# Kernel optimization log

Hardware: AMD Instinct MI355X
Metric: run time of the kernel (lower is better)

The kernel has to match this reference:

```python
import jax, jax.numpy as jnp
import numpy as np


def phi(x):
    return jax.nn.elu(x) + 1.0


def setup_inputs() -> dict:
    key = jax.random.key(0)
    ks = jax.random.split(key, 6)
    B, C, H, W = 16, 256, 64, 64
    scale = 1.0 / np.sqrt(C)
    x = jax.random.normal(ks[0], (B, C, H, W), dtype=jnp.float32)
    Wq = jax.random.normal(ks[1], (C, C), dtype=jnp.float32) * scale
    Wk = jax.random.normal(ks[2], (C, C), dtype=jnp.float32) * scale
    Wv = jax.random.normal(ks[3], (C, C), dtype=jnp.float32) * scale
    Wo = jax.random.normal(ks[4], (C, C), dtype=jnp.float32) * scale
    bo = jnp.zeros((C,), dtype=jnp.float32)
    return {"x": x, "Wq": Wq, "Wk": Wk, "Wv": Wv, "Wo": Wo, "bo": bo}


def reference(x, Wq, Wk, Wv, Wo, bo):
    # 1x1 convs == channel matmuls: out[b,o,h,w] = sum_c W[o,c] x[b,c,h,w]
    q = jnp.einsum('oc,bchw->bohw', Wq, x)
    k = jnp.einsum('oc,bchw->bohw', Wk, x)
    v = jnp.einsum('oc,bchw->bohw', Wv, x)
    phi_q, phi_k, phi_v = phi(q), phi(k), phi(v)
    # context matrix per batch: [B, C, C]
    qv = jnp.einsum('bchw,bdhw->bcd', phi_q, phi_v)
    # per-batch 1x1 conv with weight qv[b] applied to phi_k[b]
    attended = jnp.einsum('bcd,bdhw->bchw', qv, phi_k)
    # output projection with bias; dropout is identity at eval
    out = jnp.einsum('oc,bchw->bohw', Wo, attended) + bo[None, :, None, None]
    return out
```

## Files before the change

### kernel.cpp

```cpp
#include <hip/hip_runtime.h>
#include <hip/hip_bf16.h>


typedef short  bf16x8 __attribute__((ext_vector_type(8)));
typedef float  f32x4  __attribute__((ext_vector_type(4)));
typedef unsigned short u16x4 __attribute__((ext_vector_type(4)));

#define NB 16
#define NC 256
#define NN 4096

__device__ __forceinline__ unsigned short f2bf(float f) {
    union { float f; unsigned u; } v; v.f = f;
    unsigned r = v.u + 0x7FFFu + ((v.u >> 16) & 1u);
    return (unsigned short)(r >> 16);
}

__device__ __forceinline__ float phi_act(float v) {
    return v > 0.f ? v + 1.f : __expf(v);
}

__device__ __forceinline__ void gload_lds16(const void* g, void* l) {
    __builtin_amdgcn_global_load_lds(
        (const __attribute__((address_space(1))) void*)g,
        (__attribute__((address_space(3))) void*)l, 16, 0, 0);
}

__device__ __forceinline__ void stage_tile(
    const unsigned short* __restrict__ src, int ld, int kb, char* lds, int t)
{
    const int kslot  = t & 7;
    const int rbase  = t >> 3;
    const int srcOff = (kslot * 16) ^ ((rbase & 7) << 4);
    const int wbase  = (t >> 6) * 1024;
    #pragma unroll
    for (int i = 0; i < 4; ++i) {
        const int r = i * 32 + rbase;
        const char* g = (const char*)(src + (size_t)r * ld + kb) + srcOff;
        gload_lds16(g, lds + i * 4096 + wbase);
    }
}

__device__ __forceinline__ bf16x8 frag_ld(const char* lds, int row, int kbyte) {
    return *(const bf16x8*)(lds + row * 128 + (kbyte ^ ((row & 7) << 4)));
}

template<bool SWAP>
__device__ __forceinline__ void gemm_projx(
    const unsigned short* __restrict__ A,
    const float* __restrict__ xb,
    char* lsA, char* lsB, f32x4 (&acc)[4][4])
{
    const int t = threadIdx.x, lane = t & 63, w = t >> 6;
    const int wr = (w >> 1) * 64, wc = (w & 1) * 64;
    const int q = lane >> 4, c15 = lane & 15;
    const int cb = t & 15;
    const int nb0 = t >> 4;

    for (int kt = 0; kt < 4; ++kt) {
        const int kb = kt * 64;
        f32x4 bv[2][4];
        #pragma unroll
        for (int i = 0; i < 2; ++i) {
            const float* src = xb + (size_t)(kb + cb * 4) * NN + (nb0 + 16 * i) * 4;
            #pragma unroll
            for (int j = 0; j < 4; ++j)
                bv[i][j] = *(const f32x4*)(src + (size_t)j * NN);
        }
        if (kt) __syncthreads();
        stage_tile(A, NC, kb, lsA, t);
        #pragma unroll
        for (int i = 0; i < 2; ++i) {
            const int nb = nb0 + 16 * i;
            #pragma unroll
            for (int jj = 0; jj < 4; ++jj) {
                const int n = nb * 4 + jj;
                u16x4 wv;
                #pragma unroll
                for (int j = 0; j < 4; ++j) wv[j] = f2bf(bv[i][j][jj]);
                *(u16x4*)(lsB + n * 128 + ((cb * 8) ^ ((n & 7) << 4))) = wv;
            }
        }
        __syncthreads();
        #pragma unroll
        for (int g = 0; g < 2; ++g) {
            const int kbyte = g * 64 + q * 16;
            bf16x8 af[4], bfr[4];
            #pragma unroll
            for (int m = 0; m < 4; ++m) af[m]  = frag_ld(lsA, wr + m * 16 + c15, kbyte);
            #pragma unroll
            for (int n = 0; n < 4; ++n) bfr[n] = frag_ld(lsB, wc + n * 16 + c15, kbyte);
            #pragma unroll
            for (int m = 0; m < 4; ++m)
                #pragma unroll
                for (int n = 0; n < 4; ++n)
                    acc[m][n] = SWAP
                        ? __builtin_amdgcn_mfma_f32_16x16x32_bf16(bfr[n], af[m], acc[m][n], 0, 0, 0)
                        : __builtin_amdgcn_mfma_f32_16x16x32_bf16(af[m], bfr[n], acc[m][n], 0, 0, 0);
        }
    }
}

template<bool SWAP>
__device__ __forceinline__ void gemm128(
    const unsigned short* __restrict__ A, int lda,
    const unsigned short* __restrict__ BT, int ldb,
    int k0, int nk, char* lsA, char* lsB, f32x4 (&acc)[4][4])
{
    const int t = threadIdx.x;
    const int lane = t & 63;
    const int w  = t >> 6;
    const int wr = (w >> 1) * 64, wc = (w & 1) * 64;
    const int q  = lane >> 4, c15 = lane & 15;

    for (int kt = 0; kt < nk; ++kt) {
        const int kb = k0 + kt * 64;
        if (kt) __syncthreads();
        stage_tile(A,  lda, kb, lsA, t);
        stage_tile(BT, ldb, kb, lsB, t);
        __syncthreads();
        #pragma unroll
        for (int g = 0; g < 2; ++g) {
            const int kbyte = g * 64 + q * 16;
            bf16x8 af[4], bfr[4];
            #pragma unroll
            for (int m = 0; m < 4; ++m) af[m]  = frag_ld(lsA, wr + m * 16 + c15, kbyte);
            #pragma unroll
            for (int n = 0; n < 4; ++n) bfr[n] = frag_ld(lsB, wc + n * 16 + c15, kbyte);
            #pragma unroll
            for (int m = 0; m < 4; ++m)
                #pragma unroll
                for (int n = 0; n < 4; ++n)
                    acc[m][n] = SWAP
                        ? __builtin_amdgcn_mfma_f32_16x16x32_bf16(bfr[n], af[m], acc[m][n], 0, 0, 0)
                        : __builtin_amdgcn_mfma_f32_16x16x32_bf16(af[m], bfr[n], acc[m][n], 0, 0, 0);
        }
    }
}

__global__ __launch_bounds__(256) void k_wcvt(
    const float* __restrict__ Wq, const float* __restrict__ Wk,
    const float* __restrict__ Wv, const float* __restrict__ Wo,
    unsigned short* __restrict__ Wqkv, unsigned short* __restrict__ Wob)
{
    int i = blockIdx.x * 256 + threadIdx.x;
    if      (i < 65536)  Wqkv[i] = f2bf(Wq[i]);
    else if (i < 131072) Wqkv[i] = f2bf(Wk[i - 65536]);
    else if (i < 196608) Wqkv[i] = f2bf(Wv[i - 131072]);
    else if (i < 262144) Wob[i - 196608] = f2bf(Wo[i - 196608]);
}

__global__ __launch_bounds__(256) void k_proj(
    const unsigned short* __restrict__ Wqkv, const float* __restrict__ x,
    unsigned short* __restrict__ phiQ, unsigned short* __restrict__ phiKT,
    unsigned short* __restrict__ phiV)
{
    __shared__ __align__(16) char lds[32768];
    const int bid = blockIdx.x;
    const int nt  = bid & 31;
    const int mt  = (bid >> 5) % 6;
    const int b   = bid / 192;
    const unsigned short* A = Wqkv + (size_t)mt * 128 * NC;
    const float* xb = x + (size_t)b * NC * NN + nt * 128;

    const int lane = threadIdx.x & 63;
    const int w    = threadIdx.x >> 6;
    const int wr   = (w >> 1) * 64, wc = (w & 1) * 64;
    const int q4   = (lane >> 4) * 4, c15 = lane & 15;
    const int p    = mt >> 1;

    f32x4 acc[4][4] = {};
    if (p == 1) {
        gemm_projx<false>(A, xb, lds, lds + 16384, acc);
        unsigned short* dst = phiKT + (size_t)b * NN * NC;
        const int cb = (mt & 1) * 128 + wr + q4;
        const int nb = nt * 128 + wc + c15;
        #pragma unroll
        for (int m = 0; m < 4; ++m)
            #pragma unroll
            for (int n = 0; n < 4; ++n) {
                u16x4 pk;
                #pragma unroll
                for (int i = 0; i < 4; ++i) pk[i] = f2bf(phi_act(acc[m][n][i]));
                *(u16x4*)(dst + (size_t)(nb + n * 16) * NC + cb + m * 16) = pk;
            }
    } else {
        gemm_projx<true>(A, xb, lds, lds + 16384, acc);
        unsigned short* dst = (p == 0 ? phiQ : phiV) + (size_t)b * NC * NN;
        const int ob = (mt & 1) * 128 + wr + c15;
        const int nb = nt * 128 + wc + q4;
        #pragma unroll
        for (int m = 0; m < 4; ++m)
            #pragma unroll
            for (int n = 0; n < 4; ++n) {
                u16x4 pk;
                #pragma unroll
                for (int i = 0; i < 4; ++i) pk[i] = f2bf(phi_act(acc[m][n][i]));
                *(u16x4*)(dst + (size_t)(ob + m * 16) * NN + nb + n * 16) = pk;
            }
    }
}

__global__ __launch_bounds__(256) void k_qv(
    const unsigned short* __restrict__ phiQ, const unsigned short* __restrict__ phiV,
    float* __restrict__ qvTp)
{
    __shared__ char lds[32768];
    const int bid = blockIdx.x;
    const int s = bid & 7, nt = (bid >> 3) & 1, mt = (bid >> 4) & 1, b = bid >> 5;
    const unsigned short* A  = phiQ + ((size_t)b * NC + mt * 128) * NN;
    const unsigned short* BT = phiV + ((size_t)b * NC + nt * 128) * NN;
    f32x4 acc[4][4] = {};
    gemm128<false>(A, NN, BT, NN, s * 512, 8, lds, lds + 16384, acc);

    const int lane = threadIdx.x & 63, w = threadIdx.x >> 6;
    const int wr = (w >> 1) * 64, wc = (w & 1) * 64;
    const int q4 = (lane >> 4) * 4, c15 = lane & 15;
    float* dst = qvTp + (((size_t)s * NB + b) << 16);
    const int c0 = mt * 128 + wr + q4;
    const int d0 = nt * 128 + wc + c15;
    #pragma unroll
    for (int m = 0; m < 4; ++m)
        #pragma unroll
        for (int n = 0; n < 4; ++n)
            *(f32x4*)(dst + (size_t)(d0 + n * 16) * NC + c0 + m * 16) = acc[m][n];
}

__global__ __launch_bounds__(256) void k_qvred(
    const float* __restrict__ p, unsigned short* __restrict__ qvT)
{
    const size_t i = (size_t)blockIdx.x * 256 + threadIdx.x;
    const f32x4* pv = (const f32x4*)p;
    f32x4 v = pv[i];
    #pragma unroll
    for (int s = 1; s < 8; ++s) v = v + pv[i + (size_t)s * 262144];
    u16x4 o;
    #pragma unroll
    for (int j = 0; j < 4; ++j) o[j] = f2bf(v[j]);
    ((u16x4*)qvT)[i] = o;
}

__global__ __launch_bounds__(256) void k_mproj(
    const unsigned short* __restrict__ Wob, const unsigned short* __restrict__ qvT,
    unsigned short* __restrict__ Mb)
{
    __shared__ char lds[32768];
    const int bid = blockIdx.x;
    const int nt = bid & 1, mt = (bid >> 1) & 1, b = bid >> 2;
    const unsigned short* A  = Wob + mt * 128 * NC;
    const unsigned short* BT = qvT + ((size_t)b << 16) + nt * 128 * NC;
    f32x4 acc[4][4] = {};
    gemm128<true>(A, NC, BT, NC, 0, 4, lds, lds + 16384, acc);

    const int lane = threadIdx.x & 63, w = threadIdx.x >> 6;
    const int wr = (w >> 1) * 64, wc = (w & 1) * 64;
    const int q4 = (lane >> 4) * 4, c15 = lane & 15;
    unsigned short* dst = Mb + ((size_t)b << 16);
    const int ob = mt * 128 + wr + c15;
    const int db = nt * 128 + wc + q4;
    #pragma unroll
    for (int m = 0; m < 4; ++m)
        #pragma unroll
        for (int n = 0; n < 4; ++n) {
            u16x4 pk;
            #pragma unroll
            for (int i = 0; i < 4; ++i) pk[i] = f2bf(acc[m][n][i]);
            *(u16x4*)(dst + (size_t)(ob + m * 16) * NC + db + n * 16) = pk;
        }
}

__global__ __launch_bounds__(256) void k_out(
    const unsigned short* __restrict__ Mb, const unsigned short* __restrict__ phiKT,
    const float* __restrict__ bo, float* __restrict__ out)
{
    __shared__ char lds[32768];
    const int bid = blockIdx.x;
    const int nt = bid & 31, mt = (bid >> 5) & 1, b = bid >> 6;
    const unsigned short* A  = Mb + ((size_t)b << 16) + mt * 128 * NC;
    const unsigned short* BT = phiKT + (size_t)b * NN * NC + (size_t)nt * 128 * NC;
    f32x4 acc[4][4] = {};
    gemm128<true>(A, NC, BT, NC, 0, 4, lds, lds + 16384, acc);

    const int lane = threadIdx.x & 63, w = threadIdx.x >> 6;
    const int wr = (w >> 1) * 64, wc = (w & 1) * 64;
    const int q4 = (lane >> 4) * 4, c15 = lane & 15;
    float* dst = out + (size_t)b * NC * NN;
    #pragma unroll
    for (int m = 0; m < 4; ++m) {
        const int o  = mt * 128 + wr + m * 16 + c15;
        const float bb = bo[o];
        #pragma unroll
        for (int n = 0; n < 4; ++n) {
            f32x4 v = acc[m][n];
            #pragma unroll
            for (int i = 0; i < 4; ++i) v[i] += bb;
            *(f32x4*)(dst + (size_t)o * NN + nt * 128 + wc + n * 16 + q4) = v;
        }
    }
}

extern "C" void kernel_launch(void* const* d_in, const int* in_sizes, int n_in,
                              void* d_out, int out_size, void* d_ws, size_t ws_size,
                              hipStream_t stream)
{
    (void)in_sizes; (void)n_in; (void)out_size; (void)ws_size;
    const float* x  = (const float*)d_in[0];
    const float* Wq = (const float*)d_in[1];
    const float* Wk = (const float*)d_in[2];
    const float* Wv = (const float*)d_in[3];
    const float* Wo = (const float*)d_in[4];
    const float* bo = (const float*)d_in[5];
    float* out = (float*)d_out;

    char* ws = (char*)d_ws;
    size_t off = 0;
    auto alloc = [&](size_t bytes) {
        void* p = ws + off;
        off += (bytes + 255) & ~(size_t)255;
        return p;
    };
    unsigned short* phiQ  = (unsigned short*)alloc((size_t)NB * NC * NN * 2);
    unsigned short* phiV  = (unsigned short*)alloc((size_t)NB * NC * NN * 2);
    unsigned short* phiKT = (unsigned short*)alloc((size_t)NB * NN * NC * 2);
    float*          qvTp  = (float*)alloc((size_t)8 * NB * NC * NC * 4);
    unsigned short* qvT   = (unsigned short*)alloc((size_t)NB * NC * NC * 2);
    unsigned short* Mb    = (unsigned short*)alloc((size_t)NB * NC * NC * 2);
    unsigned short* Wqkv  = (unsigned short*)alloc((size_t)768 * NC * 2);
    unsigned short* Wob   = (unsigned short*)alloc((size_t)NC * NC * 2);

    k_wcvt<<<1024, 256, 0, stream>>>(Wq, Wk, Wv, Wo, Wqkv, Wob);
    k_proj<<<3072, 256, 0, stream>>>(Wqkv, x, phiQ, phiKT, phiV);
    k_qv<<<512, 256, 0, stream>>>(phiQ, phiV, qvTp);
    k_qvred<<<1024, 256, 0, stream>>>(qvTp, qvT);
    k_mproj<<<64, 256, 0, stream>>>(Wob, qvT, Mb);
    k_out<<<1024, 256, 0, stream>>>(Mb, phiKT, bo, out);
}
```

Measured before the change: 146.8 us.

## Stage x tile once in LDS and reuse across Q/K/V projection slabs

The projection kernel now loads and converts a full 256x128 x tile to bf16 into 64KB of LDS once per block, then loops over three weight slabs (Q, K, V for one half of output channels). This replaces 3072 blocks that each re-read and re-converted x with 1024 blocks, cutting redundant global reads of fp32 x by a factor of three. It uses a new two-level XOR swizzle for the wide transposed tile. The cost is 80KB of LDS per block, which limits occupancy. The qv kernel's block index is also remapped so the k-split blocks sharing a batch are spread across the grid.

```diff
diff --git a/kernel.cpp b/kernel.cpp
--- a/kernel.cpp
+++ b/kernel.cpp
@@ -26,6 +26,7 @@
         (__attribute__((address_space(3))) void*)l, 16, 0, 0);
 }
 
+template<int NR>
 __device__ __forceinline__ void stage_tile(
     const unsigned short* __restrict__ src, int ld, int kb, char* lds, int t)
 {
@@ -34,7 +35,7 @@
     const int srcOff = (kslot * 16) ^ ((rbase & 7) << 4);
     const int wbase  = (t >> 6) * 1024;
     #pragma unroll
-    for (int i = 0; i < 4; ++i) {
+    for (int i = 0; i < NR / 32; ++i) {
         const int r = i * 32 + rbase;
         const char* g = (const char*)(src + (size_t)r * ld + kb) + srcOff;
         gload_lds16(g, lds + i * 4096 + wbase);
@@ -45,42 +46,28 @@
     return *(const bf16x8*)(lds + row * 128 + (kbyte ^ ((row & 7) << 4)));
 }
 
+__device__ __forceinline__ bf16x8 fragB_ld(const char* lds, int n, int kbyte) {
+    const int fo = ((n & 7) << 4) ^ ((n & 24) << 1);
+    return *(const bf16x8*)(lds + n * 512 + (kbyte ^ fo));
+}
+
 template<bool SWAP>
-__device__ __forceinline__ void gemm_projx(
-    const unsigned short* __restrict__ A,
-    const float* __restrict__ xb,
-    char* lsA, char* lsB, f32x4 (&acc)[4][4])
-{
-    const int t = threadIdx.x, lane = t & 63, w = t >> 6;
-    const int wr = (w >> 1) * 64, wc = (w & 1) * 64;
-    const int q = lane >> 4, c15 = lane & 15;
-    const int cb = t & 15;
-    const int nb0 = t >> 4;
-
-    for (int kt = 0; kt < 4; ++kt) {
-        const int kb = kt * 64;
-        f32x4 bv[2][4];
-        #pragma unroll
-        for (int i = 0; i < 2; ++i) {
-            const float* src = xb + (size_t)(kb + cb * 4) * NN + (nb0 + 16 * i) * 4;
-            #pragma unroll
-            for (int j = 0; j < 4; ++j)
-                bv[i][j] = *(const f32x4*)(src + (size_t)j * NN);
-        }
+__device__ __forceinline__ void gemm128(
+    const unsigned short* __restrict__ A, int lda,
+    const unsigned short* __restrict__ BT, int ldb,
+    int k0, int nk, char* lsA, char* lsB, f32x4 (&acc)[4][4])
+{
+    const int t = threadIdx.x;
+    const int lane = t & 63;
+    const int w  = t >> 6;
+    const int wr = (w >> 1) * 64, wc = (w & 1) * 64;
+    const int q  = lane >> 4, c15 = lane & 15;
+
+    for (int kt = 0; kt < nk; ++kt) {
+        const int kb = k0 + kt * 64;
         if (kt) __syncthreads();
-        stage_tile(A, NC, kb, lsA, t);
-        #pragma unroll
-        for (int i = 0; i < 2; ++i) {
-            const int nb = nb0 + 16 * i;
-            #pragma unroll
-            for (int jj = 0; jj < 4; ++jj) {
-                const int n = nb * 4 + jj;
-                u16x4 wv;
-                #pragma unroll
-                for (int j = 0; j < 4; ++j) wv[j] = f2bf(bv[i][j][jj]);
-                *(u16x4*)(lsB + n * 128 + ((cb * 8) ^ ((n & 7) << 4))) = wv;
-            }
-        }
+        stage_tile<128>(A,  lda, kb, lsA, t);
+        stage_tile<128>(BT, ldb, kb, lsB, t);
         __syncthreads();
         #pragma unroll
         for (int g = 0; g < 2; ++g) {
@@ -101,43 +88,6 @@
     }
 }
 
-template<bool SWAP>
-__device__ __forceinline__ void gemm128(
-    const unsigned short* __restrict__ A, int lda,
-    const unsigned short* __restrict__ BT, int ldb,
-    int k0, int nk, char* lsA, char* lsB, f32x4 (&acc)[4][4])
-{
-    const int t = threadIdx.x;
-    const int lane = t & 63;
-    const int w  = t >> 6;
-    const int wr = (w >> 1) * 64, wc = (w & 1) * 64;
-    const int q  = lane >> 4, c15 = lane & 15;
-
-    for (int kt = 0; kt < nk; ++kt) {
-        const int kb = k0 + kt * 64;
-        if (kt) __syncthreads();
-        stage_tile(A,  lda, kb, lsA, t);
-        stage_tile(BT, ldb, kb, lsB, t);
-        __syncthreads();
-        #pragma unroll
-        for (int g = 0; g < 2; ++g) {
-            const int kbyte = g * 64 + q * 16;
-            bf16x8 af[4], bfr[4];
-            #pragma unroll
-            for (int m = 0; m < 4; ++m) af[m]  = frag_ld(lsA, wr + m * 16 + c15, kbyte);
-            #pragma unroll
-            for (int n = 0; n < 4; ++n) bfr[n] = frag_ld(lsB, wc + n * 16 + c15, kbyte);
-            #pragma unroll
-            for (int m = 0; m < 4; ++m)
-                #pragma unroll
-                for (int n = 0; n < 4; ++n)
-                    acc[m][n] = SWAP
-                        ? __builtin_amdgcn_mfma_f32_16x16x32_bf16(bfr[n], af[m], acc[m][n], 0, 0, 0)
-                        : __builtin_amdgcn_mfma_f32_16x16x32_bf16(af[m], bfr[n], acc[m][n], 0, 0, 0);
-        }
-    }
-}
-
 __global__ __launch_bounds__(256) void k_wcvt(
     const float* __restrict__ Wq, const float* __restrict__ Wk,
     const float* __restrict__ Wv, const float* __restrict__ Wo,
@@ -150,54 +100,102 @@
     else if (i < 262144) Wob[i - 196608] = f2bf(Wo[i - 196608]);
 }
 
-__global__ __launch_bounds__(256) void k_proj(
+__global__ __launch_bounds__(256) void k_projm(
     const unsigned short* __restrict__ Wqkv, const float* __restrict__ x,
     unsigned short* __restrict__ phiQ, unsigned short* __restrict__ phiKT,
     unsigned short* __restrict__ phiV)
 {
-    __shared__ __align__(16) char lds[32768];
+    __shared__ __align__(16) char lds[81920];
+    char* xTl = lds;
+    char* lsA = lds + 65536;
     const int bid = blockIdx.x;
-    const int nt  = bid & 31;
-    const int mt  = (bid >> 5) % 6;
-    const int b   = bid / 192;
-    const unsigned short* A = Wqkv + (size_t)mt * 128 * NC;
+    const int nt = bid & 31, ph = (bid >> 5) & 1, b = bid >> 6;
     const float* xb = x + (size_t)b * NC * NN + nt * 128;
-
-    const int lane = threadIdx.x & 63;
-    const int w    = threadIdx.x >> 6;
-    const int wr   = (w >> 1) * 64, wc = (w & 1) * 64;
-    const int q4   = (lane >> 4) * 4, c15 = lane & 15;
-    const int p    = mt >> 1;
-
-    f32x4 acc[4][4] = {};
-    if (p == 1) {
-        gemm_projx<false>(A, xb, lds, lds + 16384, acc);
-        unsigned short* dst = phiKT + (size_t)b * NN * NC;
-        const int cb = (mt & 1) * 128 + wr + q4;
-        const int nb = nt * 128 + wc + c15;
-        #pragma unroll
-        for (int m = 0; m < 4; ++m)
-            #pragma unroll
-            for (int n = 0; n < 4; ++n) {
-                u16x4 pk;
-                #pragma unroll
-                for (int i = 0; i < 4; ++i) pk[i] = f2bf(phi_act(acc[m][n][i]));
-                *(u16x4*)(dst + (size_t)(nb + n * 16) * NC + cb + m * 16) = pk;
+    const int t = threadIdx.x;
+
+    {
+        const int n4 = (t & 31) * 4;
+        const int c0 = t >> 5;
+        #pragma unroll 4
+        for (int cc = 0; cc < 32; ++cc) {
+            const int c = cc * 8 + c0;
+            f32x4 v = *(const f32x4*)(xb + (size_t)c * NN + n4);
+            #pragma unroll
+            for (int i = 0; i < 4; ++i) {
+                const int n = n4 + i;
+                const int fo = ((n & 7) << 4) ^ ((n & 24) << 1);
+                *(unsigned short*)(xTl + n * 512 + ((2 * c) ^ fo)) = f2bf(v[i]);
             }
-    } else {
-        gemm_projx<true>(A, xb, lds, lds + 16384, acc);
-        unsigned short* dst = (p == 0 ? phiQ : phiV) + (size_t)b * NC * NN;
-        const int ob = (mt & 1) * 128 + wr + c15;
-        const int nb = nt * 128 + wc + q4;
-        #pragma unroll
-        for (int m = 0; m < 4; ++m)
-            #pragma unroll
-            for (int n = 0; n < 4; ++n) {
-                u16x4 pk;
-                #pragma unroll
-                for (int i = 0; i < 4; ++i) pk[i] = f2bf(phi_act(acc[m][n][i]));
-                *(u16x4*)(dst + (size_t)(ob + m * 16) * NN + nb + n * 16) = pk;
+        }
+    }
+
+    const int lane = t & 63, w = t >> 6;
+    const int wr = (w >> 1) * 64, wc = (w & 1) * 64;
+    const int q = lane >> 4, c15 = lane & 15;
+    const int q4 = q * 4;
+
+    #pragma unroll
+    for (int slab = 0; slab < 3; ++slab) {
+        const int mt = slab * 2 + ph;
+        const unsigned short* A = Wqkv + (size_t)mt * 128 * NC;
+        f32x4 acc[4][4] = {};
+        for (int kt = 0; kt < 4; ++kt) {
+            __syncthreads();
+            stage_tile<128>(A, NC, kt * 64, lsA, t);
+            __syncthreads();
+            #pragma unroll
+            for (int g = 0; g < 2; ++g) {
+                const int ka = g * 64 + q * 16;
+                const int kb = kt * 128 + ka;
+                bf16x8 af[4], bfr[4];
+                #pragma unroll
+                for (int m = 0; m < 4; ++m) af[m]  = frag_ld(lsA, wr + m * 16 + c15, ka);
+                #pragma unroll
+                for (int n = 0; n < 4; ++n) bfr[n] = fragB_ld(xTl, wc + n * 16 + c15, kb);
+                if (slab == 1) {
+                    #pragma unroll
+                    for (int m = 0; m < 4; ++m)
+                        #pragma unroll
+                        for (int n = 0; n < 4; ++n)
+                            acc[m][n] = __builtin_amdgcn_mfma_f32_16x16x32_bf16(
+                                af[m], bfr[n], acc[m][n], 0, 0, 0);
+                } else {
+                    #pragma unroll
+                    for (int m = 0; m < 4; ++m)
+                        #pragma unroll
+                        for (int n = 0; n < 4; ++n)
+                            acc[m][n] = __builtin_amdgcn_mfma_f32_16x16x32_bf16(
+                                bfr[n], af[m], acc[m][n], 0, 0, 0);
+                }
             }
+        }
+        if (slab == 1) {
+            unsigned short* dst = phiKT + (size_t)b * NN * NC;
+            const int cb = ph * 128 + wr + q4;
+            const int nb = nt * 128 + wc + c15;
+            #pragma unroll
+            for (int m = 0; m < 4; ++m)
+                #pragma unroll
+                for (int n = 0; n < 4; ++n) {
+                    u16x4 pk;
+                    #pragma unroll
+                    for (int i = 0; i < 4; ++i) pk[i] = f2bf(phi_act(acc[m][n][i]));
+                    *(u16x4*)(dst + (size_t)(nb + n * 16) * NC + cb + m * 16) = pk;
+                }
+        } else {
+            unsigned short* dst = (slab == 0 ? phiQ : phiV) + (size_t)b * NC * NN;
+            const int ob = ph * 128 + wr + c15;
+            const int nb = nt * 128 + wc + q4;
+            #pragma unroll
+            for (int m = 0; m < 4; ++m)
+                #pragma unroll
+                for (int n = 0; n < 4; ++n) {
+                    u16x4 pk;
+                    #pragma unroll
+                    for (int i = 0; i < 4; ++i) pk[i] = f2bf(phi_act(acc[m][n][i]));
+                    *(u16x4*)(dst + (size_t)(ob + m * 16) * NN + nb + n * 16) = pk;
+                }
+        }
     }
 }
 
@@ -206,7 +204,7 @@
     float* __restrict__ qvTp)
 {
     __shared__ char lds[32768];
-    const int bid = blockIdx.x;
+    const int bid = (blockIdx.x & 7) * 64 + (blockIdx.x >> 3);
     const int s = bid & 7, nt = (bid >> 3) & 1, mt = (bid >> 4) & 1, b = bid >> 5;
     const unsigned short* A  = phiQ + ((size_t)b * NC + mt * 128) * NN;
     const unsigned short* BT = phiV + ((size_t)b * NC + nt * 128) * NN;
@@ -329,7 +327,7 @@
     unsigned short* Wob   = (unsigned short*)alloc((size_t)NC * NC * 2);
 
     k_wcvt<<<1024, 256, 0, stream>>>(Wq, Wk, Wv, Wo, Wqkv, Wob);
-    k_proj<<<3072, 256, 0, stream>>>(Wqkv, x, phiQ, phiKT, phiV);
+    k_projm<<<1024, 256, 0, stream>>>(Wqkv, x, phiQ, phiKT, phiV);
     k_qv<<<512, 256, 0, stream>>>(phiQ, phiV, qvTp);
     k_qvred<<<1024, 256, 0, stream>>>(qvTp, qvT);
     k_mproj<<<64, 256, 0, stream>>>(Wob, qvT, Mb);
```

After: 122.9 us. 16.3% less time.

## Stage fp32 x via async LDS loads, store bf16 partials, remap block order

Applied to the files above, without the earlier changes.

The projection kernel now copies fp32 x tiles straight into a larger swizzled LDS buffer with global_load_lds and converts them to bf16 while building MFMA fragments, instead of loading into registers, converting, and writing to LDS. The split-K partial context matrices are stored as bf16 rather than fp32, which halves the partial-buffer traffic between k_qv and k_qvred at some accuracy cost. Block indices in k_qv and k_out are permuted so that consecutive hardware blocks are spread across the XCDs. The larger LDS footprint may reduce occupancy, and the per-element LDS reads during conversion add instructions.

```diff
diff --git a/kernel.cpp b/kernel.cpp
--- a/kernel.cpp
+++ b/kernel.cpp
@@ -16,6 +16,11 @@
     return (unsigned short)(r >> 16);
 }
 
+__device__ __forceinline__ float bf2f(unsigned short h) {
+    union { unsigned u; float f; } v; v.u = (unsigned)h << 16;
+    return v.f;
+}
+
 __device__ __forceinline__ float phi_act(float v) {
     return v > 0.f ? v + 1.f : __expf(v);
 }
@@ -43,62 +48,6 @@
 
 __device__ __forceinline__ bf16x8 frag_ld(const char* lds, int row, int kbyte) {
     return *(const bf16x8*)(lds + row * 128 + (kbyte ^ ((row & 7) << 4)));
-}
-
-template<bool SWAP>
-__device__ __forceinline__ void gemm_projx(
-    const unsigned short* __restrict__ A,
-    const float* __restrict__ xb,
-    char* lsA, char* lsB, f32x4 (&acc)[4][4])
-{
-    const int t = threadIdx.x, lane = t & 63, w = t >> 6;
-    const int wr = (w >> 1) * 64, wc = (w & 1) * 64;
-    const int q = lane >> 4, c15 = lane & 15;
-    const int cb = t & 15;
-    const int nb0 = t >> 4;
-
-    for (int kt = 0; kt < 4; ++kt) {
-        const int kb = kt * 64;
-        f32x4 bv[2][4];
-        #pragma unroll
-        for (int i = 0; i < 2; ++i) {
-            const float* src = xb + (size_t)(kb + cb * 4) * NN + (nb0 + 16 * i) * 4;
-            #pragma unroll
-            for (int j = 0; j < 4; ++j)
-                bv[i][j] = *(const f32x4*)(src + (size_t)j * NN);
-        }
-        if (kt) __syncthreads();
-        stage_tile(A, NC, kb, lsA, t);
-        #pragma unroll
-        for (int i = 0; i < 2; ++i) {
-            const int nb = nb0 + 16 * i;
-            #pragma unroll
-            for (int jj = 0; jj < 4; ++jj) {
-                const int n = nb * 4 + jj;
-                u16x4 wv;
-                #pragma unroll
-                for (int j = 0; j < 4; ++j) wv[j] = f2bf(bv[i][j][jj]);
-                *(u16x4*)(lsB + n * 128 + ((cb * 8) ^ ((n & 7) << 4))) = wv;
-            }
-        }
-        __syncthreads();
-        #pragma unroll
-        for (int g = 0; g < 2; ++g) {
-            const int kbyte = g * 64 + q * 16;
-            bf16x8 af[4], bfr[4];
-            #pragma unroll
-            for (int m = 0; m < 4; ++m) af[m]  = frag_ld(lsA, wr + m * 16 + c15, kbyte);
-            #pragma unroll
-            for (int n = 0; n < 4; ++n) bfr[n] = frag_ld(lsB, wc + n * 16 + c15, kbyte);
-            #pragma unroll
-            for (int m = 0; m < 4; ++m)
-                #pragma unroll
-                for (int n = 0; n < 4; ++n)
-                    acc[m][n] = SWAP
-                        ? __builtin_amdgcn_mfma_f32_16x16x32_bf16(bfr[n], af[m], acc[m][n], 0, 0, 0)
-                        : __builtin_amdgcn_mfma_f32_16x16x32_bf16(af[m], bfr[n], acc[m][n], 0, 0, 0);
-        }
-    }
 }
 
 template<bool SWAP>
@@ -138,6 +87,58 @@
     }
 }
 
+template<bool SWAP>
+__device__ __forceinline__ void gemm_projx(
+    const unsigned short* __restrict__ A,
+    const float* __restrict__ xb,
+    char* lsA, char* lsB, f32x4 (&acc)[4][4])
+{
+    const int t = threadIdx.x, lane = t & 63, w = t >> 6;
+    const int wr = (w >> 1) * 64, wc = (w & 1) * 64;
+    const int q = lane >> 4, c15 = lane & 15;
+    const int wbase = w * 1024;
+
+    for (int kt = 0; kt < 4; ++kt) {
+        if (kt) __syncthreads();
+        stage_tile(A, NC, kt * 64, lsA, t);
+        #pragma unroll
+        for (int i = 0; i < 8; ++i) {
+            const int u    = i * 256 + t;
+            const int row  = u >> 5;
+            const int slot = u & 31;
+            const char* g = (const char*)(xb + (size_t)(kt * 64 + row) * NN)
+                          + ((slot * 16) ^ ((row & 24) << 1));
+            gload_lds16(g, lsB + i * 4096 + wbase);
+        }
+        __syncthreads();
+        #pragma unroll
+        for (int g2 = 0; g2 < 2; ++g2) {
+            const int c0 = g2 * 32 + q * 8;
+            bf16x8 af[4], bfr[4];
+            #pragma unroll
+            for (int m = 0; m < 4; ++m)
+                af[m] = frag_ld(lsA, wr + m * 16 + c15, g2 * 64 + q * 16);
+            #pragma unroll
+            for (int f = 0; f < 4; ++f) {
+                const int nn = wc + f * 16 + c15;
+                const char* bb = lsB + c0 * 512 + ((nn * 4) ^ ((c0 & 24) << 1));
+                union { bf16x8 v; unsigned short e[8]; } pk;
+                #pragma unroll
+                for (int j = 0; j < 8; ++j)
+                    pk.e[j] = f2bf(*(const float*)(bb + j * 512));
+                bfr[f] = pk.v;
+            }
+            #pragma unroll
+            for (int m = 0; m < 4; ++m)
+                #pragma unroll
+                for (int n = 0; n < 4; ++n)
+                    acc[m][n] = SWAP
+                        ? __builtin_amdgcn_mfma_f32_16x16x32_bf16(bfr[n], af[m], acc[m][n], 0, 0, 0)
+                        : __builtin_amdgcn_mfma_f32_16x16x32_bf16(af[m], bfr[n], acc[m][n], 0, 0, 0);
+        }
+    }
+}
+
 __global__ __launch_bounds__(256) void k_wcvt(
     const float* __restrict__ Wq, const float* __restrict__ Wk,
     const float* __restrict__ Wv, const float* __restrict__ Wo,
@@ -155,7 +156,7 @@
     unsigned short* __restrict__ phiQ, unsigned short* __restrict__ phiKT,
     unsigned short* __restrict__ phiV)
 {
-    __shared__ __align__(16) char lds[32768];
+    __shared__ __align__(16) char lds[49152];
     const int bid = blockIdx.x;
     const int nt  = bid & 31;
     const int mt  = (bid >> 5) % 6;
@@ -203,10 +204,10 @@
 
 __global__ __launch_bounds__(256) void k_qv(
     const unsigned short* __restrict__ phiQ, const unsigned short* __restrict__ phiV,
-    float* __restrict__ qvTp)
+    unsigned short* __restrict__ qvTp)
 {
     __shared__ char lds[32768];
-    const int bid = blockIdx.x;
+    const int bid = (blockIdx.x & 7) * 64 + (blockIdx.x >> 3);
     const int s = bid & 7, nt = (bid >> 3) & 1, mt = (bid >> 4) & 1, b = bid >> 5;
     const unsigned short* A  = phiQ + ((size_t)b * NC + mt * 128) * NN;
     const unsigned short* BT = phiV + ((size_t)b * NC + nt * 128) * NN;
@@ -216,24 +217,32 @@
     const int lane = threadIdx.x & 63, w = threadIdx.x >> 6;
     const int wr = (w >> 1) * 64, wc = (w & 1) * 64;
     const int q4 = (lane >> 4) * 4, c15 = lane & 15;
-    float* dst = qvTp + (((size_t)s * NB + b) << 16);
+    unsigned short* dst = qvTp + (((size_t)s * NB + b) << 16);
     const int c0 = mt * 128 + wr + q4;
     const int d0 = nt * 128 + wc + c15;
     #pragma unroll
     for (int m = 0; m < 4; ++m)
         #pragma unroll
-        for (int n = 0; n < 4; ++n)
-            *(f32x4*)(dst + (size_t)(d0 + n * 16) * NC + c0 + m * 16) = acc[m][n];
+        for (int n = 0; n < 4; ++n) {
+            u16x4 pk;
+            #pragma unroll
+            for (int i = 0; i < 4; ++i) pk[i] = f2bf(acc[m][n][i]);
+            *(u16x4*)(dst + (size_t)(d0 + n * 16) * NC + c0 + m * 16) = pk;
+        }
 }
 
 __global__ __launch_bounds__(256) void k_qvred(
-    const float* __restrict__ p, unsigned short* __restrict__ qvT)
+    const unsigned short* __restrict__ p, unsigned short* __restrict__ qvT)
 {
     const size_t i = (size_t)blockIdx.x * 256 + threadIdx.x;
-    const f32x4* pv = (const f32x4*)p;
-    f32x4 v = pv[i];
-    #pragma unroll
-    for (int s = 1; s < 8; ++s) v = v + pv[i + (size_t)s * 262144];
+    const u16x4* pv = (const u16x4*)p;
+    f32x4 v = {0.f, 0.f, 0.f, 0.f};
+    #pragma unroll
+    for (int s = 0; s < 8; ++s) {
+        u16x4 a = pv[i + (size_t)s * 262144];
+        #pragma unroll
+        for (int j = 0; j < 4; ++j) v[j] += bf2f(a[j]);
+    }
     u16x4 o;
     #pragma unroll
     for (int j = 0; j < 4; ++j) o[j] = f2bf(v[j]);
@@ -274,7 +283,7 @@
     const float* __restrict__ bo, float* __restrict__ out)
 {
     __shared__ char lds[32768];
-    const int bid = blockIdx.x;
+    const int bid = (blockIdx.x & 7) * 128 + (blockIdx.x >> 3);
     const int nt = bid & 31, mt = (bid >> 5) & 1, b = bid >> 6;
     const unsigned short* A  = Mb + ((size_t)b << 16) + mt * 128 * NC;
     const unsigned short* BT = phiKT + (size_t)b * NN * NC + (size_t)nt * 128 * NC;
@@ -322,7 +331,7 @@
     unsigned short* phiQ  = (unsigned short*)alloc((size_t)NB * NC * NN * 2);
     unsigned short* phiV  = (unsigned short*)alloc((size_t)NB * NC * NN * 2);
     unsigned short* phiKT = (unsigned short*)alloc((size_t)NB * NN * NC * 2);
-    float*          qvTp  = (float*)alloc((size_t)8 * NB * NC * NC * 4);
+    unsigned short* qvTp  = (unsigned short*)alloc((size_t)8 * NB * NC * NC * 2);
     unsigned short* qvT   = (unsigned short*)alloc((size_t)NB * NC * NC * 2);
     unsigned short* Mb    = (unsigned short*)alloc((size_t)NB * NC * NC * 2);
     unsigned short* Wqkv  = (unsigned short*)alloc((size_t)768 * NC * 2);
```

Result: faster. 134.5 us (-8.3%).
